# Kernel tuning notes

Hardware: AMD Instinct MI355X
Metric: run time of the kernel (lower is better)

## Reference

```python
import jax, jax.numpy as jnp
import numpy as np

# MUCMA: multiuser CMA adaptive MIMO FIR equalizer (commplax af.mucma)
# framed_signal: (N, taps, dims) complex, carried as re/im float32 pairs.
N, TAPS, DIMS, DELTA = 131072, 19, 2, 6
LR = 2.0 ** (-13)
BETA = 0.999
R2 = 1.32  # E|a|^4 / E|a|^2 for unit-power 16QAM constellation


def setup_inputs() -> dict:
    key = jax.random.key(0)
    k1, k2 = jax.random.split(key)
    fr_re = jax.random.normal(k1, (N, TAPS, DIMS), dtype=jnp.float32) * 0.7071
    fr_im = jax.random.normal(k2, (N, TAPS, DIMS), dtype=jnp.float32) * 0.7071
    # initial MIMO weights: identity at the center tap (commplax mucma init)
    w0_re = np.zeros((DIMS, DIMS, TAPS), dtype=np.float32)
    ctap = (TAPS + 1) // 2 - 1
    w0_re[np.arange(DIMS), np.arange(DIMS), ctap] = 1.0
    return {
        'fr_re': fr_re,
        'fr_im': fr_im,
        'w0_re': jnp.asarray(w0_re),
        'w0_im': jnp.zeros((DIMS, DIMS, TAPS), jnp.float32),
    }


def _mucma_forward(fr_re, fr_im, w0_re, w0_im):
    u_all = fr_re + 1j * fr_im                      # (N, taps, dims) complex64
    w0 = (w0_re + 1j * w0_im).astype(u_all.dtype)   # (dims, dims, taps)
    # mask kills self cross-correlation terms (k == l)
    mask = (1.0 - jnp.eye(DIMS, dtype=jnp.float32))[:, :, None]

    def step(carry, u):
        # u: (taps, dims) frame of input samples
        w, z, r, bp = carry
        v = jnp.einsum('ijt,tj->i', w, u)                     # MIMO FIR output, (dims,)
        z = jnp.concatenate((v[None, :], z[:-1]))             # output delay line, (delta, dims)
        # running cross-correlation r[k,l,d] ~ E[z_k(n) z_l(n-d)^*]
        r = BETA * r + (1.0 - BETA) * jnp.einsum('k,dl->kld', v, z.conj())
        rhat = (r / (1.0 - bp)) * mask                        # bias-corrected, off-diagonal only
        e = R2 - jnp.abs(v) ** 2                              # CMA modulus error, (dims,) real
        loss = jnp.sum(e ** 2) + 2.0 * jnp.sum(jnp.abs(rhat) ** 2)
        uc = u.conj().T[None, :, :]                           # (1, dims, taps)
        g_cma = -2.0 * e[:, None, None] * v[:, None, None] * uc
        g_mu = 2.0 * jnp.einsum('kld,dl->k', rhat, z.conj())[:, None, None] * uc
        w_new = w - LR * (g_cma + g_mu)
        bp = bp * BETA
        # emit the weights USED for this symbol (pre-update), as commplax does
        return (w_new, z, r, bp), (w, loss)

    z0 = jnp.zeros((DELTA, DIMS), u_all.dtype)
    r0 = jnp.zeros((DIMS, DIMS, DELTA), u_all.dtype)
    carry0 = (w0, z0, r0, jnp.float32(BETA))
    _, (ws, _losses) = jax.lax.scan(step, carry0, u_all)
    # apply: per-symbol MIMO filtering with the recorded weight trace
    sig = jnp.einsum('nijt,ntj->ni', ws, u_all)               # (N, dims) complex
    return jnp.stack([sig.real, sig.imag], axis=-1)           # (N, dims, 2) float32


def reference(fr_re, fr_im, w0_re, w0_im):
    return _mucma_forward(fr_re, fr_im, w0_re, w0_im)
```

## Files before the change

### kernel.cpp

```cpp
#include <hip/hip_runtime.h>


typedef float v2f __attribute__((ext_vector_type(2)));

constexpr int   NTAPS  = 19;
constexpr int   FRST   = 38;
constexpr float BETA_C = 0.999f;
constexpr float OMB_C  = 0.001f;
constexpr float LR_C   = 0.0001220703125f;
constexpr float R2_C   = 1.32f;

template <int CTRL, int RMASK = 0xF>
__device__ __forceinline__ float dpp_add(float x) {
    return x + __int_as_float(__builtin_amdgcn_update_dpp(
        0, __float_as_int(x), CTRL, RMASK, 0xF, true));
}
template <int CTRL>
__device__ __forceinline__ float dpp_mov(float x) {
    return __int_as_float(__builtin_amdgcn_update_dpp(
        0, __float_as_int(x), CTRL, 0xF, 0xF, true));
}
__device__ __forceinline__ float bperm(int addr, float x) {
    return __int_as_float(__builtin_amdgcn_ds_bpermute(addr, __float_as_int(x)));
}
__device__ __forceinline__ float halfred(float x) {
    x = dpp_add<0x111>(x);
    x = dpp_add<0x112>(x);
    x = dpp_add<0x114>(x);
    x = dpp_add<0x118>(x);
    x = dpp_add<0x142, 0xA>(x);
    return x;
}
__device__ __forceinline__ float qsum8(float x) {
    x = dpp_add<0x111>(x);
    x = dpp_add<0x112>(x);
    x = dpp_add<0x114>(x);
    return x;
}

__global__ void __launch_bounds__(64, 1)
mucma_scan_kernel(const float* __restrict__ fr_re, const float* __restrict__ fr_im,
                  const float* __restrict__ w0r_in, const float* __restrict__ w0i_in,
                  float* __restrict__ out, int nsym)
{
    const int   lane  = threadIdx.x;
    const int   s     = lane & 31;
    const int   dim   = lane >> 5;
    const int   smin  = (s < NTAPS) ? s : (NTAPS - 1);
    const float act   = (s < NTAPS) ? 1.0f : 0.0f;
    const int   addrA = 4 * (dim ? 63 : 31);
    const int   addrB = 4 * (dim ? 31 : 63);
    const bool  d0f   = (s == 24);
    const float qmask = (s >= 24 && s < 30) ? 1.0f : 0.0f;
    const bool  is_st = ((lane & 31) == 0);

    v2f w_r = {0.f, 0.f}, w_i = {0.f, 0.f};
    if (s < NTAPS) {
        w_r.x = w0r_in[dim * FRST + s];
        w_r.y = w0r_in[dim * FRST + NTAPS + s];
        w_i.x = w0i_in[dim * FRST + s];
        w_i.y = w0i_in[dim * FRST + NTAPS + s];
    }
    float r_re = 0.f, r_im = 0.f, z_re = 0.f, z_im = 0.f;
    float bp = BETA_C;

    const int uo = 2 * smin;

    v2f rr[8], ri[8];
#pragma unroll
    for (int p = 0; p < 8; ++p) {
        const int idx = (p < nsym) ? p : (nsym - 1);
        rr[p] = *(const v2f*)(fr_re + idx * FRST + uo);
        ri[p] = *(const v2f*)(fr_im + idx * FRST + uo);
    }

    auto body = [&](int n, int p, int npf) {
        const v2f ur = rr[p], ui = ri[p];
        rr[p] = *(const v2f*)(fr_re + (size_t)npf * FRST + uo);
        ri[p] = *(const v2f*)(fr_im + (size_t)npf * FRST + uo);

        const v2f prv = w_r * ur - w_i * ui;
        const v2f piv = w_r * ui + w_i * ur;
        float xr = prv.x + prv.y;
        float xi = piv.x + piv.y;
        xr = halfred(xr);
        xi = halfred(xi);
        const float vkr = bperm(addrA, xr);
        const float vki = bperm(addrA, xi);
        const float vlr = bperm(addrB, xr);
        const float vli = bperm(addrB, xi);

        const float zsr = dpp_mov<0x111>(z_re);
        const float zsi = dpp_mov<0x111>(z_im);
        z_re = d0f ? vlr : zsr;
        z_im = d0f ? vli : zsi;

        const float ar = OMB_C * vkr, ai = OMB_C * vki;
        r_re = BETA_C * r_re + (ar * z_re + ai * z_im);
        r_im = BETA_C * r_im + (ai * z_re - ar * z_im);

        float qr = (r_re * z_re + r_im * z_im) * qmask;
        float qi = (r_im * z_re - r_re * z_im) * qmask;
        qr = qsum8(qr);
        qi = qsum8(qi);

        const float inv = __builtin_amdgcn_rcpf(1.0f - bp);
        bp *= BETA_C;
        const float i2  = (2.0f * LR_C) * inv;
        const float ek  = R2_C - (vkr * vkr + vki * vki);
        const float ek2 = (-2.0f * LR_C) * ek;
        const float crv = ek2 * vkr + i2 * qr;
        const float civ = ek2 * vki + i2 * qi;
        const float ccr = bperm(addrA, crv) * act;
        const float cci = bperm(addrA, civ) * act;

        const v2f c_r = {ccr, ccr};
        const v2f c_i = {cci, cci};
        w_r = w_r - c_r * ur - c_i * ui;
        w_i = w_i - c_i * ur + c_r * ui;

        if (is_st) {
            v2f o; o.x = vkr; o.y = vki;
            *(v2f*)(out + 4 * (size_t)n + 2 * dim) = o;
        }
    };

    int NBmain = nsym / 8 - 1;
    if (NBmain < 0) NBmain = 0;
    for (int b = 0; b < NBmain; ++b) {
        const int nb = b * 8;
#pragma unroll
        for (int p = 0; p < 8; ++p) body(nb + p, p, nb + p + 8);
    }
    for (int nb = NBmain * 8; nb < nsym; nb += 8) {
#pragma unroll
        for (int p = 0; p < 8; ++p) {
            const int n = nb + p;
            if (n < nsym) {
                int npf = n + 8;
                if (npf > nsym - 1) npf = nsym - 1;
                body(n, p, npf);
            }
        }
    }
}

extern "C" void kernel_launch(void* const* d_in, const int* in_sizes, int n_in,
                              void* d_out, int out_size, void* d_ws, size_t ws_size,
                              hipStream_t stream)
{
    const float* fr_re = (const float*)d_in[0];
    const float* fr_im = (const float*)d_in[1];
    const float* w0r   = (const float*)d_in[2];
    const float* w0i   = (const float*)d_in[3];
    float* outp = (float*)d_out;
    const int nsym = in_sizes[0] / FRST;
    hipLaunchKernelGGL(mucma_scan_kernel, dim3(1), dim3(64), 0, stream,
                       fr_re, fr_im, w0r, w0i, outp, nsym);
}
```

Measured before the change: 27.76 ms.

## Pack two taps per lane and replace bpermute with row DPP and permlane32 swap

Remaps the data so each lane holds two taps. The FIR reduction for one output then fits inside a 16-lane DPP row broadcast, and the cross-half exchange uses v_permlane32_swap instead of ds_bpermute. The coefficient broadcast bpermute is removed, since every lane in the row already holds the reduced values. This shortens the serial per-symbol dependency chain, which is the cost of this single-wave scan. The trade-off is more FMAs per lane, wider unaligned 16-byte loads, and reliance on gfx950-specific permlane semantics, which are checked at runtime through csel.

```diff
diff --git a/kernel.cpp b/kernel.cpp
--- a/kernel.cpp
+++ b/kernel.cpp
@@ -2,6 +2,7 @@
 
 
 typedef float v2f __attribute__((ext_vector_type(2)));
+typedef float v4f __attribute__((ext_vector_type(4), aligned(4)));
 
 constexpr int   NTAPS  = 19;
 constexpr int   FRST   = 38;
@@ -10,32 +11,28 @@
 constexpr float LR_C   = 0.0001220703125f;
 constexpr float R2_C   = 1.32f;
 
-template <int CTRL, int RMASK = 0xF>
+template <int CTRL>
 __device__ __forceinline__ float dpp_add(float x) {
     return x + __int_as_float(__builtin_amdgcn_update_dpp(
-        0, __float_as_int(x), CTRL, RMASK, 0xF, true));
+        0, __float_as_int(x), CTRL, 0xF, 0xF, true));
 }
 template <int CTRL>
 __device__ __forceinline__ float dpp_mov(float x) {
     return __int_as_float(__builtin_amdgcn_update_dpp(
         0, __float_as_int(x), CTRL, 0xF, 0xF, true));
 }
-__device__ __forceinline__ float bperm(int addr, float x) {
-    return __int_as_float(__builtin_amdgcn_ds_bpermute(addr, __float_as_int(x)));
-}
-__device__ __forceinline__ float halfred(float x) {
-    x = dpp_add<0x111>(x);
-    x = dpp_add<0x112>(x);
-    x = dpp_add<0x114>(x);
-    x = dpp_add<0x118>(x);
-    x = dpp_add<0x142, 0xA>(x);
+__device__ __forceinline__ float rowred_bcast(float x) {
+    x = dpp_add<0x121>(x);
+    x = dpp_add<0x122>(x);
+    x = dpp_add<0x124>(x);
+    x = dpp_add<0x128>(x);
     return x;
 }
-__device__ __forceinline__ float qsum8(float x) {
-    x = dpp_add<0x111>(x);
-    x = dpp_add<0x112>(x);
-    x = dpp_add<0x114>(x);
-    return x;
+__device__ __forceinline__ void plane32_swap(float& a, float& b) {
+    asm("s_nop 1\n\t"
+        "v_permlane32_swap_b32 %0, %1\n\t"
+        "s_nop 1"
+        : "+v"(a), "+v"(b));
 }
 
 __global__ void __launch_bounds__(64, 1)
@@ -43,52 +40,69 @@
                   const float* __restrict__ w0r_in, const float* __restrict__ w0i_in,
                   float* __restrict__ out, int nsym)
 {
-    const int   lane  = threadIdx.x;
-    const int   s     = lane & 31;
-    const int   dim   = lane >> 5;
-    const int   smin  = (s < NTAPS) ? s : (NTAPS - 1);
-    const float act   = (s < NTAPS) ? 1.0f : 0.0f;
-    const int   addrA = 4 * (dim ? 63 : 31);
-    const int   addrB = 4 * (dim ? 31 : 63);
-    const bool  d0f   = (s == 24);
-    const float qmask = (s >= 24 && s < 30) ? 1.0f : 0.0f;
-    const bool  is_st = ((lane & 31) == 0);
+    const int  lane = threadIdx.x;
+    const int  sl   = lane & 31;
+    const int  h    = lane >> 5;
+    const int  loff = (4 * sl < 34) ? 4 * sl : 34;
+    const float mA  = (sl <= 8) ? 1.f : 0.f;
+    const float mB  = (sl <= 9) ? 1.f : 0.f;
+    const bool d0f  = (sl == 10);
+    const bool stf  = (sl == 0);
 
-    v2f w_r = {0.f, 0.f}, w_i = {0.f, 0.f};
-    if (s < NTAPS) {
-        w_r.x = w0r_in[dim * FRST + s];
-        w_r.y = w0r_in[dim * FRST + NTAPS + s];
-        w_i.x = w0i_in[dim * FRST + s];
-        w_i.y = w0i_in[dim * FRST + NTAPS + s];
+    v2f wA_r = {0.f,0.f}, wA_i = {0.f,0.f}, wB_r = {0.f,0.f}, wB_i = {0.f,0.f};
+    if (sl <= 8) {
+        const int b = h * FRST + 2 * sl;
+        wA_r.x = w0r_in[b];         wA_r.y = w0r_in[b + NTAPS];
+        wA_i.x = w0i_in[b];         wA_i.y = w0i_in[b + NTAPS];
+        wB_r.x = w0r_in[b + 1];     wB_r.y = w0r_in[b + NTAPS + 1];
+        wB_i.x = w0i_in[b + 1];     wB_i.y = w0i_in[b + NTAPS + 1];
+    } else if (sl == 9) {
+        wB_r.x = w0r_in[h * FRST + 18];  wB_r.y = w0r_in[h * FRST + 37];
+        wB_i.x = w0i_in[h * FRST + 18];  wB_i.y = w0i_in[h * FRST + 37];
     }
     float r_re = 0.f, r_im = 0.f, z_re = 0.f, z_im = 0.f;
     float bp = BETA_C;
 
-    const int uo = 2 * smin;
+    bool csel;
+    {
+        const float own = h ? 11.f : 7.f;
+        float v = own, X = own;
+        plane32_swap(X, v);
+        csel = (X != own);
+    }
 
-    v2f rr[8], ri[8];
+    const float* pre = fr_re + loff;
+    const float* pim = fr_im + loff;
+
+    v4f rr[8], ri[8];
 #pragma unroll
     for (int p = 0; p < 8; ++p) {
         const int idx = (p < nsym) ? p : (nsym - 1);
-        rr[p] = *(const v2f*)(fr_re + idx * FRST + uo);
-        ri[p] = *(const v2f*)(fr_im + idx * FRST + uo);
+        rr[p] = *(const v4f*)(pre + (size_t)idx * FRST);
+        ri[p] = *(const v4f*)(pim + (size_t)idx * FRST);
     }
 
     auto body = [&](int n, int p, int npf) {
-        const v2f ur = rr[p], ui = ri[p];
-        rr[p] = *(const v2f*)(fr_re + (size_t)npf * FRST + uo);
-        ri[p] = *(const v2f*)(fr_im + (size_t)npf * FRST + uo);
+        const v4f uR = rr[p], uI = ri[p];
+        rr[p] = *(const v4f*)(pre + (size_t)npf * FRST);
+        ri[p] = *(const v4f*)(pim + (size_t)npf * FRST);
 
-        const v2f prv = w_r * ur - w_i * ui;
-        const v2f piv = w_r * ui + w_i * ur;
-        float xr = prv.x + prv.y;
-        float xi = piv.x + piv.y;
-        xr = halfred(xr);
-        xi = halfred(xi);
-        const float vkr = bperm(addrA, xr);
-        const float vki = bperm(addrA, xi);
-        const float vlr = bperm(addrB, xr);
-        const float vli = bperm(addrB, xi);
+        const v2f uA_r = {uR.x, uR.y}, uB_r = {uR.z, uR.w};
+        const v2f uA_i = {uI.x, uI.y}, uB_i = {uI.z, uI.w};
+
+        v2f tr = wA_r * uA_r - wA_i * uA_i + wB_r * uB_r - wB_i * uB_i;
+        v2f ti = wA_r * uA_i + wA_i * uA_r + wB_r * uB_i + wB_i * uB_r;
+        float xr = tr.x + tr.y;
+        float xi = ti.x + ti.y;
+        xr = rowred_bcast(xr);
+        xi = rowred_bcast(xi);
+        const float vkr = xr, vki = xi;
+
+        float Xr = xr, Xi = xi;
+        plane32_swap(Xr, xr);
+        plane32_swap(Xi, xi);
+        const float vlr = csel ? Xr : xr;
+        const float vli = csel ? Xi : xi;
 
         const float zsr = dpp_mov<0x111>(z_re);
         const float zsi = dpp_mov<0x111>(z_im);
@@ -99,29 +113,31 @@
         r_re = BETA_C * r_re + (ar * z_re + ai * z_im);
         r_im = BETA_C * r_im + (ai * z_re - ar * z_im);
 
-        float qr = (r_re * z_re + r_im * z_im) * qmask;
-        float qi = (r_im * z_re - r_re * z_im) * qmask;
-        qr = qsum8(qr);
-        qi = qsum8(qi);
+        float qr = r_re * z_re + r_im * z_im;
+        float qi = r_im * z_re - r_re * z_im;
+        qr = rowred_bcast(qr);
+        qi = rowred_bcast(qi);
 
         const float inv = __builtin_amdgcn_rcpf(1.0f - bp);
         bp *= BETA_C;
-        const float i2  = (2.0f * LR_C) * inv;
-        const float ek  = R2_C - (vkr * vkr + vki * vki);
-        const float ek2 = (-2.0f * LR_C) * ek;
-        const float crv = ek2 * vkr + i2 * qr;
-        const float civ = ek2 * vki + i2 * qi;
-        const float ccr = bperm(addrA, crv) * act;
-        const float cci = bperm(addrA, civ) * act;
+        const float i2 = (2.0f * LR_C) * inv;
+        const float ek = R2_C - (vkr * vkr + vki * vki);
+        const float e2 = (-2.0f * LR_C) * ek;
+        const float cr = e2 * vkr + i2 * qr;
+        const float ci = e2 * vki + i2 * qi;
 
-        const v2f c_r = {ccr, ccr};
-        const v2f c_i = {cci, cci};
-        w_r = w_r - c_r * ur - c_i * ui;
-        w_i = w_i - c_i * ur + c_r * ui;
+        const float crA = cr * mA, ciA = ci * mA;
+        const float crB = cr * mB, ciB = ci * mB;
+        const v2f cAr = {crA, crA}, cAi = {ciA, ciA};
+        const v2f cBr = {crB, crB}, cBi = {ciB, ciB};
+        wA_r -= cAr * uA_r + cAi * uA_i;
+        wA_i -= cAi * uA_r - cAr * uA_i;
+        wB_r -= cBr * uB_r + cBi * uB_i;
+        wB_i -= cBi * uB_r - cBr * uB_i;
 
-        if (is_st) {
+        if (stf) {
             v2f o; o.x = vkr; o.y = vki;
-            *(v2f*)(out + 4 * (size_t)n + 2 * dim) = o;
+            *(v2f*)(out + 4 * (size_t)n + 2 * h) = o;
         }
     };
 
```

After: 29.79 ms. +7.3%, slower.
